# Performance work log

Hardware: AMD Instinct MI355X
Metric: run time of the kernel (lower is better)

Reference implementation:

```python
import jax, jax.numpy as jnp
import numpy as np

D = 768
HEAD_SIZE = 64  # D // 12


def setup_inputs() -> dict:
    key = jax.random.key(0)
    k_ix, k_wk, k_wq, k_wv = jax.random.split(key, 4)
    ix = jax.random.normal(k_ix, (4, 4096, D), dtype=jnp.float32)
    s = 1.0 / np.sqrt(D)
    Wk = jax.random.normal(k_wk, (D, HEAD_SIZE), dtype=jnp.float32) * s
    Wq = jax.random.normal(k_wq, (D, HEAD_SIZE), dtype=jnp.float32) * s
    Wv = jax.random.normal(k_wv, (D, HEAD_SIZE), dtype=jnp.float32) * s
    return {"ix": ix, "Wk": Wk, "Wq": Wq, "Wv": Wv}


def reference(ix, Wk, Wq, Wv):
    # ix: [B, N, D]; W*: [D, h]
    k = ix @ Wk            # [B, N, h]
    q = ix @ Wq            # [B, N, h]
    v = ix @ Wv            # [B, N, h]
    scale = HEAD_SIZE ** -0.5
    wei = jnp.einsum('bnh,bmh->bnm', q, k) * scale  # [B, N, N]
    wei = jax.nn.softmax(wei, axis=-1)
    out = jnp.einsum('bnm,bmh->bnh', wei, v)        # [B, N, h]
    return out
```

## Files before the change

### kernel.cpp

```cpp
#include <hip/hip_runtime.h>
#include <math.h>

#define Dm   768
#define Hm   64
#define SEQ  4096
#define NB   4
#define NROW (NB * SEQ)

#define QSCALE (0.125f * 1.4426950408889634f)

typedef _Float16 f16;
typedef __attribute__((ext_vector_type(8))) _Float16 f16x8;
typedef __attribute__((ext_vector_type(2))) __fp16 fp16x2_raw;
typedef __attribute__((ext_vector_type(4))) float f32x4;
typedef unsigned int uint;
typedef unsigned short ushort;

#define MFMAH(A, B, C) __builtin_amdgcn_mfma_f32_16x16x32_f16(A, B, C, 0, 0, 0)

__device__ __forceinline__ uint pkrtz(float a, float b) {
    fp16x2_raw r = __builtin_amdgcn_cvt_pkrtz(a, b);
    return __builtin_bit_cast(uint, r);
}
__device__ __forceinline__ ushort f2h(float f) {
    f16 h = (f16)f;
    return __builtin_bit_cast(ushort, h);
}
union F16x8U { uint u[4]; f16x8 v; };

__global__ __launch_bounds__(256) void wconv(
    const float* __restrict__ Wq, const float* __restrict__ Wk,
    const float* __restrict__ Wv, ushort* __restrict__ WTt)
{
    const int c   = blockIdx.x;
    const int mat = c >> 6, col = c & 63;
    const float* W = (mat == 0) ? Wq : (mat == 1 ? Wk : Wv);
    const float sc = (mat == 0) ? QSCALE : 1.0f;
    for (int k = threadIdx.x; k < Dm; k += 256)
        WTt[((size_t)(k >> 5) * 192 + c) * 32 + (k & 31)] = f2h(W[k * 64 + col] * sc);
}

__global__ __launch_bounds__(256, 3) void proj(
    const float* __restrict__ ix, const ushort* __restrict__ WTt,
    ushort* __restrict__ Qw, ushort* __restrict__ Kt, ushort* __restrict__ Vt)
{
    __shared__ __align__(16) float comb[2][3072];

    const int t    = threadIdx.x;
    const int lane = t & 63;
    const int kh   = __builtin_amdgcn_readfirstlane(t >> 6);
    const int q15  = lane & 15, quad = lane >> 4;
    const int gr0  = blockIdx.x * 16;

    const float*  Ab = ix + (size_t)(gr0 + q15) * Dm + kh * 192 + quad * 8;
    const ushort* Bb = WTt + ((size_t)(kh * 6) * 192 + q15) * 32 + quad * 8;

    f32x4 acc[12];
#pragma unroll
    for (int ct = 0; ct < 12; ++ct) acc[ct] = (f32x4){0.f, 0.f, 0.f, 0.f};

    f32x4 Af[3][2];
#pragma unroll
    for (int i = 0; i < 2; ++i) {
        Af[i][0] = *(const f32x4*)(Ab + i * 32);
        Af[i][1] = *(const f32x4*)(Ab + i * 32 + 4);
    }

#pragma unroll
    for (int it = 0; it < 6; ++it) {
        f16x8 Bf[12];
#pragma unroll
        for (int ct = 0; ct < 12; ++ct)
            Bf[ct] = *(const f16x8*)(Bb + (size_t)it * 6144 + ct * 512);

        if (it + 2 < 6) {
            Af[(it + 2) % 3][0] = *(const f32x4*)(Ab + (it + 2) * 32);
            Af[(it + 2) % 3][1] = *(const f32x4*)(Ab + (it + 2) * 32 + 4);
        }

        F16x8U af;
        af.u[0] = pkrtz(Af[it % 3][0].x, Af[it % 3][0].y);
        af.u[1] = pkrtz(Af[it % 3][0].z, Af[it % 3][0].w);
        af.u[2] = pkrtz(Af[it % 3][1].x, Af[it % 3][1].y);
        af.u[3] = pkrtz(Af[it % 3][1].z, Af[it % 3][1].w);
        __builtin_amdgcn_s_setprio(1);
#pragma unroll
        for (int ct = 0; ct < 12; ++ct)
            acc[ct] = MFMAH(af.v, Bf[ct], acc[ct]);
        __builtin_amdgcn_s_setprio(0);
    }

    if (kh >= 2) {
#pragma unroll
        for (int ct = 0; ct < 12; ++ct)
            *(f32x4*)&comb[kh - 2][(ct * 64 + lane) * 4] = acc[ct];
    }
    __syncthreads();
    if (kh < 2) {
#pragma unroll
        for (int ct = 0; ct < 12; ++ct) {
            f32x4 o = *(const f32x4*)&comb[kh][(ct * 64 + lane) * 4];
            acc[ct].x += o.x; acc[ct].y += o.y; acc[ct].z += o.z; acc[ct].w += o.w;
        }
    }
    __syncthreads();
    if (kh == 1) {
#pragma unroll
        for (int ct = 0; ct < 12; ++ct)
            *(f32x4*)&comb[0][(ct * 64 + lane) * 4] = acc[ct];
    }
    __syncthreads();
    if (kh == 0) {
#pragma unroll
        for (int ct = 0; ct < 12; ++ct) {
            f32x4 o = *(const f32x4*)&comb[0][(ct * 64 + lane) * 4];
            acc[ct].x += o.x; acc[ct].y += o.y; acc[ct].z += o.z; acc[ct].w += o.w;
        }
        const int h16 = (gr0 >> 4) & 1;
        const int n4  = gr0 >> 4;
        const int j32 = gr0 >> 5;
#pragma unroll
        for (int ct = 0; ct < 12; ++ct) {
            float vals[4] = {acc[ct].x, acc[ct].y, acc[ct].z, acc[ct].w};
            if (ct < 4) {
#pragma unroll
                for (int r = 0; r < 4; ++r)
                    Qw[(size_t)(gr0 + quad * 4 + r) * 64 + ct * 16 + q15] = f2h(vals[r]);
            } else if (ct < 8) {
#pragma unroll
                for (int r = 0; r < 4; ++r)
                    Kt[(size_t)n4 * 1024 + (ct - 4) * 256 + (quad * 4 + r) * 16 + q15] = f2h(vals[r]);
            } else {
                ushort4 vv;
                vv.x = f2h(vals[0]); vv.y = f2h(vals[1]);
                vv.z = f2h(vals[2]); vv.w = f2h(vals[3]);
                *(ushort4*)(Vt + (size_t)j32 * 2048 + (ct - 8) * 512 +
                            (h16 * 2 + (quad >> 1)) * 128 + q15 * 8 + (quad & 1) * 4) = vv;
            }
        }
    }
}

#define OSTR 68
#define OBUF 4352

__global__ __launch_bounds__(512, 2) void attn(
    const ushort* __restrict__ Qw, const ushort* __restrict__ Kt,
    const ushort* __restrict__ Vt, float* __restrict__ out)
{
    __shared__ __align__(16) float aF[20992];
    short* aS = (short*)aF;

    const int t    = threadIdx.x;
    const int lane = t & 63;
    const int w    = __builtin_amdgcn_readfirstlane(t >> 6);
    const int q15  = lane & 15, quad = lane >> 4;

    const int bb    = blockIdx.x;
    const int xcd   = bb & 7;
    const int batch = xcd >> 1;
    const int slot  = (bb >> 3) | ((xcd & 1) << 5);
    const int q0    = slot * 64;
    const size_t base = (size_t)batch * SEQ;

    f16x8 qf[4][2];
#pragma unroll
    for (int g = 0; g < 4; ++g)
#pragma unroll
        for (int h = 0; h < 2; ++h)
            qf[g][h] = *(const f16x8*)(Qw + (base + q0 + g * 16 + q15) * 64 + h * 32 + quad * 8);

    f32x4 oacc[4][4];
#pragma unroll
    for (int g = 0; g < 4; ++g)
#pragma unroll
        for (int dt = 0; dt < 4; ++dt) oacc[g][dt] = (f32x4){0.f, 0.f, 0.f, 0.f};
    float lsum[4] = {0.f, 0.f, 0.f, 0.f};

    const size_t j0g = base + w * 512;
    const ushort* Kfb = Kt + (j0g >> 4) * 1024;
    const ushort* Vfb = Vt + (j0g >> 5) * 2048 + lane * 8;
    short* Ps = aS + w * 5120;

    int koff[2][2];
#pragma unroll
    for (int jt = 0; jt < 2; ++jt)
#pragma unroll
        for (int h = 0; h < 2; ++h)
            koff[jt][h] = jt * 1024 + h * 512 + (quad >> 1) * 256 + q15 * 16 + (quad & 1) * 8;

    f16x8 kf[3][2][2], vf[3][4];

#define LOADKV(slotc, i)                                                       \
    {                                                                          \
        _Pragma("unroll") for (int jt = 0; jt < 2; ++jt)                       \
        _Pragma("unroll") for (int h = 0; h < 2; ++h)                          \
            kf[slotc][jt][h] = *(const f16x8*)(Kfb + (size_t)(i) * 2048 + koff[jt][h]); \
        _Pragma("unroll") for (int dt = 0; dt < 4; ++dt)                       \
            vf[slotc][dt] = *(const f16x8*)(Vfb + (size_t)(i) * 2048 + dt * 512); \
    }
#define QKSTEP(slotc, pb)                                                      \
    {                                                                          \
        _Pragma("unroll") for (int g = 0; g < 4; ++g)                          \
        _Pragma("unroll") for (int jt = 0; jt < 2; ++jt) {                     \
            f32x4 z = (f32x4){0.f, 0.f, 0.f, 0.f};                             \
            z = MFMAH(kf[slotc][jt][0], qf[g][0], z);                          \
            z = MFMAH(kf[slotc][jt][1], qf[g][1], z);                          \
            float e0 = exp2f(z.x), e1 = exp2f(z.y);                            \
            float e2 = exp2f(z.z), e3 = exp2f(z.w);                            \
            lsum[g] += (e0 + e1) + (e2 + e3);                                  \
            uint2 pk = make_uint2(pkrtz(e0, e1), pkrtz(e2, e3));               \
            *(uint2*)(Ps + (pb) * 2560 + (g * 16 + q15) * 40 + jt * 16 + quad * 4) = pk; \
        }                                                                      \
    }
#define PVSTEP(slotc, pb)                                                      \
    {                                                                          \
        f16x8 pf[4];                                                           \
        _Pragma("unroll") for (int g = 0; g < 4; ++g)                          \
            pf[g] = *(const f16x8*)(Ps + (pb) * 2560 + (g * 16 + q15) * 40 + quad * 8); \
        __builtin_amdgcn_s_setprio(1);                                         \
        _Pragma("unroll") for (int dt = 0; dt < 4; ++dt)                       \
        _Pragma("unroll") for (int g = 0; g < 4; ++g)                          \
            oacc[g][dt] = MFMAH(pf[g], vf[slotc][dt], oacc[g][dt]);            \
        __builtin_amdgcn_s_setprio(0);                                         \
    }

    LOADKV(0, 0);
    LOADKV(1, 1);
    QKSTEP(0, 0);
#pragma unroll
    for (int i = 0; i < 16; ++i) {
        if (i + 2 < 16) LOADKV((i + 2) % 3, i + 2);
        if (i + 1 < 16) QKSTEP((i + 1) % 3, (i + 1) & 1);
        PVSTEP(i % 3, i & 1);
    }

#pragma unroll
    for (int g = 0; g < 4; ++g) {
        lsum[g] += __shfl_xor(lsum[g], 16);
        lsum[g] += __shfl_xor(lsum[g], 32);
    }
    if (quad == 0) {
#pragma unroll
        for (int g = 0; g < 4; ++g)
            aF[20480 + w * 64 + g * 16 + q15] = lsum[g];
    }
    __syncthreads();

#define OWRITE(idx)                                                          \
    {                                                                        \
        float* b = aF + (idx) * OBUF;                                        \
        _Pragma("unroll") for (int g = 0; g < 4; ++g)                        \
        _Pragma("unroll") for (int dt = 0; dt < 4; ++dt) {                   \
            b[(g * 16 + quad * 4 + 0) * OSTR + dt * 16 + q15] = oacc[g][dt].x; \
            b[(g * 16 + quad * 4 + 1) * OSTR + dt * 16 + q15] = oacc[g][dt].y; \
            b[(g * 16 + quad * 4 + 2) * OSTR + dt * 16 + q15] = oacc[g][dt].z; \
            b[(g * 16 + quad * 4 + 3) * OSTR + dt * 16 + q15] = oacc[g][dt].w; \
        }                                                                    \
    }
#define OADD(idx)                                                            \
    {                                                                        \
        const float* b = aF + (idx) * OBUF;                                  \
        _Pragma("unroll") for (int g = 0; g < 4; ++g)                        \
        _Pragma("unroll") for (int dt = 0; dt < 4; ++dt) {                   \
            oacc[g][dt].x += b[(g * 16 + quad * 4 + 0) * OSTR + dt * 16 + q15];\
            oacc[g][dt].y += b[(g * 16 + quad * 4 + 1) * OSTR + dt * 16 + q15];\
            oacc[g][dt].z += b[(g * 16 + quad * 4 + 2) * OSTR + dt * 16 + q15];\
            oacc[g][dt].w += b[(g * 16 + quad * 4 + 3) * OSTR + dt * 16 + q15];\
        }                                                                    \
    }
    if (w >= 4) OWRITE(w - 4);
    __syncthreads();
    if (w < 4) OADD(w);
    __syncthreads();
    if (w == 2 || w == 3) OWRITE(w - 2);
    __syncthreads();
    if (w < 2) OADD(w);
    __syncthreads();
    if (w < 2) OWRITE(w);
    __syncthreads();

    {
        const int q  = t >> 3;
        const int d0 = (t & 7) * 8;
        float l = 0.f;
#pragma unroll
        for (int i = 0; i < 8; ++i) l += aF[20480 + i * 64 + q];
        const float linv = 1.0f / l;
#pragma unroll
        for (int k2 = 0; k2 < 2; ++k2) {
            float4 a = *(const float4*)&aF[q * OSTR + d0 + k2 * 4];
            float4 b = *(const float4*)&aF[OBUF + q * OSTR + d0 + k2 * 4];
            float4 s;
            s.x = (a.x + b.x) * linv; s.y = (a.y + b.y) * linv;
            s.z = (a.z + b.z) * linv; s.w = (a.w + b.w) * linv;
            *(float4*)(out + (base + q0 + q) * 64 + d0 + k2 * 4) = s;
        }
    }
}

extern "C" void kernel_launch(void* const* d_in, const int* in_sizes, int n_in,
                              void* d_out, int out_size, void* d_ws, size_t ws_size,
                              hipStream_t stream)
{
    const float* ix = (const float*)d_in[0];
    const float* Wk = (const float*)d_in[1];
    const float* Wq = (const float*)d_in[2];
    const float* Wv = (const float*)d_in[3];
    float* out = (float*)d_out;

    ushort* Qw  = (ushort*)d_ws;
    ushort* Kt  = Qw + (size_t)NROW * Hm;
    ushort* Vt  = Kt + (size_t)NROW * Hm;
    ushort* WTt = Vt + (size_t)NROW * Hm;

    wconv<<<192, 256, 0, stream>>>(Wq, Wk, Wv, WTt);
    proj<<<1024, 256, 0, stream>>>(ix, WTt, Qw, Kt, Vt);
    attn<<<256, 512, 0, stream>>>(Qw, Kt, Vt, out);
}
```

Before: 135.4 us.

## Fuse weight conversion, projection and attention into one cooperative kernel

Merges the three kernels (weight conversion, QKV projection, attention) into a single cooperative launch of 256 blocks, with grid-wide syncs between phases. The projection phase is rebuilt so each 512-thread block handles 64 rows, using four row groups split across two K-halves, instead of 16 rows per 256-thread block. The aim is to remove two kernel launch gaps and per-launch tail effects. The cost is grid-sync overhead, only 256 blocks doing projection with a longer serial K loop per wave, and occupancy now bounded by the attention kernel's launch bounds and shared memory.

```diff
diff --git a/kernel.cpp b/kernel.cpp
--- a/kernel.cpp
+++ b/kernel.cpp
@@ -1,5 +1,8 @@
 #include <hip/hip_runtime.h>
+#include <hip/hip_cooperative_groups.h>
 #include <math.h>
+
+namespace cg = cooperative_groups;
 
 #define Dm   768
 #define Hm   64
@@ -28,135 +31,122 @@
 }
 union F16x8U { uint u[4]; f16x8 v; };
 
-__global__ __launch_bounds__(256) void wconv(
-    const float* __restrict__ Wq, const float* __restrict__ Wk,
-    const float* __restrict__ Wv, ushort* __restrict__ WTt)
-{
-    const int c   = blockIdx.x;
-    const int mat = c >> 6, col = c & 63;
-    const float* W = (mat == 0) ? Wq : (mat == 1 ? Wk : Wv);
-    const float sc = (mat == 0) ? QSCALE : 1.0f;
-    for (int k = threadIdx.x; k < Dm; k += 256)
-        WTt[((size_t)(k >> 5) * 192 + c) * 32 + (k & 31)] = f2h(W[k * 64 + col] * sc);
-}
-
-__global__ __launch_bounds__(256, 3) void proj(
-    const float* __restrict__ ix, const ushort* __restrict__ WTt,
-    ushort* __restrict__ Qw, ushort* __restrict__ Kt, ushort* __restrict__ Vt)
-{
-    __shared__ __align__(16) float comb[2][3072];
-
-    const int t    = threadIdx.x;
-    const int lane = t & 63;
-    const int kh   = __builtin_amdgcn_readfirstlane(t >> 6);
-    const int q15  = lane & 15, quad = lane >> 4;
-    const int gr0  = blockIdx.x * 16;
-
-    const float*  Ab = ix + (size_t)(gr0 + q15) * Dm + kh * 192 + quad * 8;
-    const ushort* Bb = WTt + ((size_t)(kh * 6) * 192 + q15) * 32 + quad * 8;
-
-    f32x4 acc[12];
-#pragma unroll
-    for (int ct = 0; ct < 12; ++ct) acc[ct] = (f32x4){0.f, 0.f, 0.f, 0.f};
-
-    f32x4 Af[3][2];
-#pragma unroll
-    for (int i = 0; i < 2; ++i) {
-        Af[i][0] = *(const f32x4*)(Ab + i * 32);
-        Af[i][1] = *(const f32x4*)(Ab + i * 32 + 4);
-    }
-
-#pragma unroll
-    for (int it = 0; it < 6; ++it) {
-        f16x8 Bf[12];
-#pragma unroll
-        for (int ct = 0; ct < 12; ++ct)
-            Bf[ct] = *(const f16x8*)(Bb + (size_t)it * 6144 + ct * 512);
-
-        if (it + 2 < 6) {
-            Af[(it + 2) % 3][0] = *(const f32x4*)(Ab + (it + 2) * 32);
-            Af[(it + 2) % 3][1] = *(const f32x4*)(Ab + (it + 2) * 32 + 4);
-        }
-
-        F16x8U af;
-        af.u[0] = pkrtz(Af[it % 3][0].x, Af[it % 3][0].y);
-        af.u[1] = pkrtz(Af[it % 3][0].z, Af[it % 3][0].w);
-        af.u[2] = pkrtz(Af[it % 3][1].x, Af[it % 3][1].y);
-        af.u[3] = pkrtz(Af[it % 3][1].z, Af[it % 3][1].w);
-        __builtin_amdgcn_s_setprio(1);
-#pragma unroll
-        for (int ct = 0; ct < 12; ++ct)
-            acc[ct] = MFMAH(af.v, Bf[ct], acc[ct]);
-        __builtin_amdgcn_s_setprio(0);
-    }
-
-    if (kh >= 2) {
-#pragma unroll
-        for (int ct = 0; ct < 12; ++ct)
-            *(f32x4*)&comb[kh - 2][(ct * 64 + lane) * 4] = acc[ct];
-    }
-    __syncthreads();
-    if (kh < 2) {
-#pragma unroll
-        for (int ct = 0; ct < 12; ++ct) {
-            f32x4 o = *(const f32x4*)&comb[kh][(ct * 64 + lane) * 4];
-            acc[ct].x += o.x; acc[ct].y += o.y; acc[ct].z += o.z; acc[ct].w += o.w;
-        }
-    }
-    __syncthreads();
-    if (kh == 1) {
-#pragma unroll
-        for (int ct = 0; ct < 12; ++ct)
-            *(f32x4*)&comb[0][(ct * 64 + lane) * 4] = acc[ct];
-    }
-    __syncthreads();
-    if (kh == 0) {
-#pragma unroll
-        for (int ct = 0; ct < 12; ++ct) {
-            f32x4 o = *(const f32x4*)&comb[0][(ct * 64 + lane) * 4];
-            acc[ct].x += o.x; acc[ct].y += o.y; acc[ct].z += o.z; acc[ct].w += o.w;
-        }
-        const int h16 = (gr0 >> 4) & 1;
-        const int n4  = gr0 >> 4;
-        const int j32 = gr0 >> 5;
-#pragma unroll
-        for (int ct = 0; ct < 12; ++ct) {
-            float vals[4] = {acc[ct].x, acc[ct].y, acc[ct].z, acc[ct].w};
-            if (ct < 4) {
-#pragma unroll
-                for (int r = 0; r < 4; ++r)
-                    Qw[(size_t)(gr0 + quad * 4 + r) * 64 + ct * 16 + q15] = f2h(vals[r]);
-            } else if (ct < 8) {
-#pragma unroll
-                for (int r = 0; r < 4; ++r)
-                    Kt[(size_t)n4 * 1024 + (ct - 4) * 256 + (quad * 4 + r) * 16 + q15] = f2h(vals[r]);
-            } else {
-                ushort4 vv;
-                vv.x = f2h(vals[0]); vv.y = f2h(vals[1]);
-                vv.z = f2h(vals[2]); vv.w = f2h(vals[3]);
-                *(ushort4*)(Vt + (size_t)j32 * 2048 + (ct - 8) * 512 +
-                            (h16 * 2 + (quad >> 1)) * 128 + q15 * 8 + (quad & 1) * 4) = vv;
-            }
-        }
-    }
-}
-
 #define OSTR 68
 #define OBUF 4352
 
-__global__ __launch_bounds__(512, 2) void attn(
-    const ushort* __restrict__ Qw, const ushort* __restrict__ Kt,
-    const ushort* __restrict__ Vt, float* __restrict__ out)
+__global__ __launch_bounds__(512, 2) void fused(
+    const float* __restrict__ ix,
+    const float* __restrict__ Wq, const float* __restrict__ Wk,
+    const float* __restrict__ Wv,
+    ushort* __restrict__ WTt,
+    ushort* __restrict__ Qw, ushort* __restrict__ Kt, ushort* __restrict__ Vt,
+    float* __restrict__ out)
 {
     __shared__ __align__(16) float aF[20992];
     short* aS = (short*)aF;
+
+    cg::grid_group grid = cg::this_grid();
 
     const int t    = threadIdx.x;
     const int lane = t & 63;
     const int w    = __builtin_amdgcn_readfirstlane(t >> 6);
     const int q15  = lane & 15, quad = lane >> 4;
-
-    const int bb    = blockIdx.x;
+    const int bb   = blockIdx.x;
+
+    if (bb < 192) {
+        const int c   = bb;
+        const int mat = c >> 6, col = c & 63;
+        const float* W = (mat == 0) ? Wq : (mat == 1 ? Wk : Wv);
+        const float sc = (mat == 0) ? QSCALE : 1.0f;
+        for (int k = t; k < Dm; k += 512)
+            WTt[((size_t)(k >> 5) * 192 + c) * 32 + (k & 31)] = f2h(W[k * 64 + col] * sc);
+    }
+    __threadfence();
+    grid.sync();
+
+    {
+        const int g   = w >> 1;
+        const int kh  = w & 1;
+        const int gr0 = bb * 64 + g * 16;
+
+        const float*  Ab = ix + (size_t)(gr0 + q15) * Dm + kh * 384 + quad * 8;
+        const ushort* Bb = WTt + ((size_t)(kh * 12) * 192 + q15) * 32 + quad * 8;
+
+        f32x4 acc[12];
+#pragma unroll
+        for (int ct = 0; ct < 12; ++ct) acc[ct] = (f32x4){0.f, 0.f, 0.f, 0.f};
+
+        f32x4 Af[3][2];
+#pragma unroll
+        for (int i = 0; i < 2; ++i) {
+            Af[i][0] = *(const f32x4*)(Ab + i * 32);
+            Af[i][1] = *(const f32x4*)(Ab + i * 32 + 4);
+        }
+
+#pragma unroll
+        for (int it = 0; it < 12; ++it) {
+            f16x8 Bf[12];
+#pragma unroll
+            for (int ct = 0; ct < 12; ++ct)
+                Bf[ct] = *(const f16x8*)(Bb + (size_t)it * 6144 + ct * 512);
+
+            if (it + 2 < 12) {
+                Af[(it + 2) % 3][0] = *(const f32x4*)(Ab + (it + 2) * 32);
+                Af[(it + 2) % 3][1] = *(const f32x4*)(Ab + (it + 2) * 32 + 4);
+            }
+
+            F16x8U af;
+            af.u[0] = pkrtz(Af[it % 3][0].x, Af[it % 3][0].y);
+            af.u[1] = pkrtz(Af[it % 3][0].z, Af[it % 3][0].w);
+            af.u[2] = pkrtz(Af[it % 3][1].x, Af[it % 3][1].y);
+            af.u[3] = pkrtz(Af[it % 3][1].z, Af[it % 3][1].w);
+            __builtin_amdgcn_s_setprio(1);
+#pragma unroll
+            for (int ct = 0; ct < 12; ++ct)
+                acc[ct] = MFMAH(af.v, Bf[ct], acc[ct]);
+            __builtin_amdgcn_s_setprio(0);
+        }
+
+        float* cb = aF + g * 3072;
+        if (kh == 1) {
+#pragma unroll
+            for (int ct = 0; ct < 12; ++ct)
+                *(f32x4*)&cb[(ct * 64 + lane) * 4] = acc[ct];
+        }
+        __syncthreads();
+        if (kh == 0) {
+#pragma unroll
+            for (int ct = 0; ct < 12; ++ct) {
+                f32x4 o = *(const f32x4*)&cb[(ct * 64 + lane) * 4];
+                acc[ct].x += o.x; acc[ct].y += o.y; acc[ct].z += o.z; acc[ct].w += o.w;
+            }
+            const int h16 = (gr0 >> 4) & 1;
+            const int n4  = gr0 >> 4;
+            const int j32 = gr0 >> 5;
+#pragma unroll
+            for (int ct = 0; ct < 12; ++ct) {
+                float vals[4] = {acc[ct].x, acc[ct].y, acc[ct].z, acc[ct].w};
+                if (ct < 4) {
+#pragma unroll
+                    for (int r = 0; r < 4; ++r)
+                        Qw[(size_t)(gr0 + quad * 4 + r) * 64 + ct * 16 + q15] = f2h(vals[r]);
+                } else if (ct < 8) {
+#pragma unroll
+                    for (int r = 0; r < 4; ++r)
+                        Kt[(size_t)n4 * 1024 + (ct - 4) * 256 + (quad * 4 + r) * 16 + q15] = f2h(vals[r]);
+                } else {
+                    ushort4 vv;
+                    vv.x = f2h(vals[0]); vv.y = f2h(vals[1]);
+                    vv.z = f2h(vals[2]); vv.w = f2h(vals[3]);
+                    *(ushort4*)(Vt + (size_t)j32 * 2048 + (ct - 8) * 512 +
+                                (h16 * 2 + (quad >> 1)) * 128 + q15 * 8 + (quad & 1) * 4) = vv;
+                }
+            }
+        }
+    }
+    __threadfence();
+    grid.sync();
+
     const int xcd   = bb & 7;
     const int batch = xcd >> 1;
     const int slot  = (bb >> 3) | ((xcd & 1) << 5);
@@ -314,7 +304,9 @@
     ushort* Vt  = Kt + (size_t)NROW * Hm;
     ushort* WTt = Vt + (size_t)NROW * Hm;
 
-    wconv<<<192, 256, 0, stream>>>(Wq, Wk, Wv, WTt);
-    proj<<<1024, 256, 0, stream>>>(ix, WTt, Qw, Kt, Vt);
-    attn<<<256, 512, 0, stream>>>(Qw, Kt, Vt, out);
+    void* args[] = {(void*)&ix, (void*)&Wq, (void*)&Wk, (void*)&Wv,
+                    (void*)&WTt, (void*)&Qw, (void*)&Kt, (void*)&Vt,
+                    (void*)&out};
+    hipLaunchCooperativeKernel((const void*)fused, dim3(256), dim3(512),
+                               args, 0, stream);
 }
```

After: 313.2 us. +131.3%, slower.

## Process two row tiles per proj block and transpose weights via LDS

Applied to the files above, without the earlier changes.

The projection kernel now handles 32 rows per block instead of 16. Each loaded weight fragment is reused across two MFMA row tiles, which halves the B-operand global loads per output, and the grid shrinks to 512 blocks. The weight-conversion kernel now transposes through a padded shared-memory tile so its global reads and writes are coalesced. In exchange, register and LDS use per block roughly double (occupancy hint drops to 2), and there are fewer blocks to spread across the CUs.

```diff
diff --git a/kernel.cpp b/kernel.cpp
--- a/kernel.cpp
+++ b/kernel.cpp
@@ -32,38 +32,56 @@
     const float* __restrict__ Wq, const float* __restrict__ Wk,
     const float* __restrict__ Wv, ushort* __restrict__ WTt)
 {
-    const int c   = blockIdx.x;
-    const int mat = c >> 6, col = c & 63;
-    const float* W = (mat == 0) ? Wq : (mat == 1 ? Wk : Wv);
-    const float sc = (mat == 0) ? QSCALE : 1.0f;
-    for (int k = threadIdx.x; k < Dm; k += 256)
-        WTt[((size_t)(k >> 5) * 192 + c) * 32 + (k & 31)] = f2h(W[k * 64 + col] * sc);
-}
-
-__global__ __launch_bounds__(256, 3) void proj(
+    __shared__ ushort lt[64 * 33];
+    const int b  = blockIdx.x;
+    const int kt = b / 3, m = b - kt * 3;
+    const float* W = (m == 0) ? Wq : (m == 1 ? Wk : Wv);
+    const float sc = (m == 0) ? QSCALE : 1.0f;
+    const int t = threadIdx.x;
+#pragma unroll
+    for (int p = 0; p < 8; ++p) {
+        int t2 = p * 256 + t;
+        int kl = t2 >> 6, c = t2 & 63;
+        lt[c * 33 + kl] = f2h(W[(size_t)(kt * 32 + kl) * 64 + c] * sc);
+    }
+    __syncthreads();
+#pragma unroll
+    for (int p = 0; p < 8; ++p) {
+        int t2 = p * 256 + t;
+        int c = t2 >> 5, kk = t2 & 31;
+        WTt[((size_t)kt * 192 + m * 64 + c) * 32 + kk] = lt[c * 33 + kk];
+    }
+}
+
+__global__ __launch_bounds__(256, 2) void proj(
     const float* __restrict__ ix, const ushort* __restrict__ WTt,
     ushort* __restrict__ Qw, ushort* __restrict__ Kt, ushort* __restrict__ Vt)
 {
-    __shared__ __align__(16) float comb[2][3072];
+    __shared__ __align__(16) float comb[2][2][3072];
 
     const int t    = threadIdx.x;
     const int lane = t & 63;
     const int kh   = __builtin_amdgcn_readfirstlane(t >> 6);
     const int q15  = lane & 15, quad = lane >> 4;
-    const int gr0  = blockIdx.x * 16;
-
-    const float*  Ab = ix + (size_t)(gr0 + q15) * Dm + kh * 192 + quad * 8;
+    const int gr0  = blockIdx.x * 32;
+
+    const float* Ab0 = ix + (size_t)(gr0 + q15) * Dm + kh * 192 + quad * 8;
+    const float* Ab1 = Ab0 + (size_t)16 * Dm;
     const ushort* Bb = WTt + ((size_t)(kh * 6) * 192 + q15) * 32 + quad * 8;
 
-    f32x4 acc[12];
-#pragma unroll
-    for (int ct = 0; ct < 12; ++ct) acc[ct] = (f32x4){0.f, 0.f, 0.f, 0.f};
-
-    f32x4 Af[3][2];
+    f32x4 acc[2][12];
+#pragma unroll
+    for (int rt = 0; rt < 2; ++rt)
+#pragma unroll
+        for (int ct = 0; ct < 12; ++ct) acc[rt][ct] = (f32x4){0.f, 0.f, 0.f, 0.f};
+
+    f32x4 Af[2][3][2];
 #pragma unroll
     for (int i = 0; i < 2; ++i) {
-        Af[i][0] = *(const f32x4*)(Ab + i * 32);
-        Af[i][1] = *(const f32x4*)(Ab + i * 32 + 4);
+        Af[0][i][0] = *(const f32x4*)(Ab0 + i * 32);
+        Af[0][i][1] = *(const f32x4*)(Ab0 + i * 32 + 4);
+        Af[1][i][0] = *(const f32x4*)(Ab1 + i * 32);
+        Af[1][i][1] = *(const f32x4*)(Ab1 + i * 32 + 4);
     }
 
 #pragma unroll
@@ -74,68 +92,88 @@
             Bf[ct] = *(const f16x8*)(Bb + (size_t)it * 6144 + ct * 512);
 
         if (it + 2 < 6) {
-            Af[(it + 2) % 3][0] = *(const f32x4*)(Ab + (it + 2) * 32);
-            Af[(it + 2) % 3][1] = *(const f32x4*)(Ab + (it + 2) * 32 + 4);
+            Af[0][(it + 2) % 3][0] = *(const f32x4*)(Ab0 + (it + 2) * 32);
+            Af[0][(it + 2) % 3][1] = *(const f32x4*)(Ab0 + (it + 2) * 32 + 4);
+            Af[1][(it + 2) % 3][0] = *(const f32x4*)(Ab1 + (it + 2) * 32);
+            Af[1][(it + 2) % 3][1] = *(const f32x4*)(Ab1 + (it + 2) * 32 + 4);
         }
 
-        F16x8U af;
-        af.u[0] = pkrtz(Af[it % 3][0].x, Af[it % 3][0].y);
-        af.u[1] = pkrtz(Af[it % 3][0].z, Af[it % 3][0].w);
-        af.u[2] = pkrtz(Af[it % 3][1].x, Af[it % 3][1].y);
-        af.u[3] = pkrtz(Af[it % 3][1].z, Af[it % 3][1].w);
+        F16x8U af0, af1;
+        af0.u[0] = pkrtz(Af[0][it % 3][0].x, Af[0][it % 3][0].y);
+        af0.u[1] = pkrtz(Af[0][it % 3][0].z, Af[0][it % 3][0].w);
+        af0.u[2] = pkrtz(Af[0][it % 3][1].x, Af[0][it % 3][1].y);
+        af0.u[3] = pkrtz(Af[0][it % 3][1].z, Af[0][it % 3][1].w);
+        af1.u[0] = pkrtz(Af[1][it % 3][0].x, Af[1][it % 3][0].y);
+        af1.u[1] = pkrtz(Af[1][it % 3][0].z, Af[1][it % 3][0].w);
+        af1.u[2] = pkrtz(Af[1][it % 3][1].x, Af[1][it % 3][1].y);
+        af1.u[3] = pkrtz(Af[1][it % 3][1].z, Af[1][it % 3][1].w);
         __builtin_amdgcn_s_setprio(1);
 #pragma unroll
-        for (int ct = 0; ct < 12; ++ct)
-            acc[ct] = MFMAH(af.v, Bf[ct], acc[ct]);
+        for (int ct = 0; ct < 12; ++ct) {
+            acc[0][ct] = MFMAH(af0.v, Bf[ct], acc[0][ct]);
+            acc[1][ct] = MFMAH(af1.v, Bf[ct], acc[1][ct]);
+        }
         __builtin_amdgcn_s_setprio(0);
     }
 
     if (kh >= 2) {
 #pragma unroll
-        for (int ct = 0; ct < 12; ++ct)
-            *(f32x4*)&comb[kh - 2][(ct * 64 + lane) * 4] = acc[ct];
+        for (int rt = 0; rt < 2; ++rt)
+#pragma unroll
+            for (int ct = 0; ct < 12; ++ct)
+                *(f32x4*)&comb[rt][kh - 2][(ct * 64 + lane) * 4] = acc[rt][ct];
     }
     __syncthreads();
     if (kh < 2) {
 #pragma unroll
-        for (int ct = 0; ct < 12; ++ct) {
-            f32x4 o = *(const f32x4*)&comb[kh][(ct * 64 + lane) * 4];
-            acc[ct].x += o.x; acc[ct].y += o.y; acc[ct].z += o.z; acc[ct].w += o.w;
-        }
+        for (int rt = 0; rt < 2; ++rt)
+#pragma unroll
+            for (int ct = 0; ct < 12; ++ct) {
+                f32x4 o = *(const f32x4*)&comb[rt][kh][(ct * 64 + lane) * 4];
+                acc[rt][ct].x += o.x; acc[rt][ct].y += o.y;
+                acc[rt][ct].z += o.z; acc[rt][ct].w += o.w;
+            }
     }
     __syncthreads();
     if (kh == 1) {
 #pragma unroll
-        for (int ct = 0; ct < 12; ++ct)
-            *(f32x4*)&comb[0][(ct * 64 + lane) * 4] = acc[ct];
+        for (int rt = 0; rt < 2; ++rt)
+#pragma unroll
+            for (int ct = 0; ct < 12; ++ct)
+                *(f32x4*)&comb[rt][0][(ct * 64 + lane) * 4] = acc[rt][ct];
     }
     __syncthreads();
     if (kh == 0) {
 #pragma unroll
-        for (int ct = 0; ct < 12; ++ct) {
-            f32x4 o = *(const f32x4*)&comb[0][(ct * 64 + lane) * 4];
-            acc[ct].x += o.x; acc[ct].y += o.y; acc[ct].z += o.z; acc[ct].w += o.w;
-        }
-        const int h16 = (gr0 >> 4) & 1;
-        const int n4  = gr0 >> 4;
-        const int j32 = gr0 >> 5;
-#pragma unroll
-        for (int ct = 0; ct < 12; ++ct) {
-            float vals[4] = {acc[ct].x, acc[ct].y, acc[ct].z, acc[ct].w};
-            if (ct < 4) {
-#pragma unroll
-                for (int r = 0; r < 4; ++r)
-                    Qw[(size_t)(gr0 + quad * 4 + r) * 64 + ct * 16 + q15] = f2h(vals[r]);
-            } else if (ct < 8) {
-#pragma unroll
-                for (int r = 0; r < 4; ++r)
-                    Kt[(size_t)n4 * 1024 + (ct - 4) * 256 + (quad * 4 + r) * 16 + q15] = f2h(vals[r]);
-            } else {
-                ushort4 vv;
-                vv.x = f2h(vals[0]); vv.y = f2h(vals[1]);
-                vv.z = f2h(vals[2]); vv.w = f2h(vals[3]);
-                *(ushort4*)(Vt + (size_t)j32 * 2048 + (ct - 8) * 512 +
-                            (h16 * 2 + (quad >> 1)) * 128 + q15 * 8 + (quad & 1) * 4) = vv;
+        for (int rt = 0; rt < 2; ++rt) {
+#pragma unroll
+            for (int ct = 0; ct < 12; ++ct) {
+                f32x4 o = *(const f32x4*)&comb[rt][0][(ct * 64 + lane) * 4];
+                acc[rt][ct].x += o.x; acc[rt][ct].y += o.y;
+                acc[rt][ct].z += o.z; acc[rt][ct].w += o.w;
+            }
+            const int gr  = gr0 + rt * 16;
+            const int n4  = gr >> 4;
+            const int h16 = n4 & 1;
+            const int j32 = gr >> 5;
+#pragma unroll
+            for (int ct = 0; ct < 12; ++ct) {
+                float vals[4] = {acc[rt][ct].x, acc[rt][ct].y, acc[rt][ct].z, acc[rt][ct].w};
+                if (ct < 4) {
+#pragma unroll
+                    for (int r = 0; r < 4; ++r)
+                        Qw[(size_t)(gr + quad * 4 + r) * 64 + ct * 16 + q15] = f2h(vals[r]);
+                } else if (ct < 8) {
+#pragma unroll
+                    for (int r = 0; r < 4; ++r)
+                        Kt[(size_t)n4 * 1024 + (ct - 4) * 256 + (quad * 4 + r) * 16 + q15] = f2h(vals[r]);
+                } else {
+                    ushort4 vv;
+                    vv.x = f2h(vals[0]); vv.y = f2h(vals[1]);
+                    vv.z = f2h(vals[2]); vv.w = f2h(vals[3]);
+                    *(ushort4*)(Vt + (size_t)j32 * 2048 + (ct - 8) * 512 +
+                                (h16 * 2 + (quad >> 1)) * 128 + q15 * 8 + (quad & 1) * 4) = vv;
+                }
             }
         }
     }
@@ -314,7 +352,7 @@
     ushort* Vt  = Kt + (size_t)NROW * Hm;
     ushort* WTt = Vt + (size_t)NROW * Hm;
 
-    wconv<<<192, 256, 0, stream>>>(Wq, Wk, Wv, WTt);
-    proj<<<1024, 256, 0, stream>>>(ix, WTt, Qw, Kt, Vt);
+    wconv<<<72, 256, 0, stream>>>(Wq, Wk, Wv, WTt);
+    proj<<<512, 256, 0, stream>>>(ix, WTt, Qw, Kt, Vt);
     attn<<<256, 512, 0, stream>>>(Qw, Kt, Vt, out);
 }
```

New measurement: 128.9 us. -4.8%, faster.
